# Kernel optimization log

Hardware: AMD Instinct MI355X
Metric: run time of the kernel (lower is better)

The kernel has to match this reference:

```python
import jax, jax.numpy as jnp
import numpy as np

B, N, D, A = 4, 4096, 512, 64

def setup_inputs() -> dict:
    key = jax.random.key(0)
    ks = jax.random.split(key, 7)
    s = 1.0 / np.sqrt(D)
    return {
        "inputs": jax.random.normal(ks[0], (B, N, D), dtype=jnp.float32),
        "Wq": jax.random.normal(ks[1], (D, A), dtype=jnp.float32) * s,
        "bq": jnp.zeros((A,), dtype=jnp.float32),
        "Wk": jax.random.normal(ks[2], (D, A), dtype=jnp.float32) * s,
        "bk": jnp.zeros((A,), dtype=jnp.float32),
        "Wv": jax.random.normal(ks[3], (D, A), dtype=jnp.float32) * s,
        "bv": jnp.zeros((A,), dtype=jnp.float32),
    }

def reference(inputs, Wq, bq, Wk, bk, Wv, bv):
    # Dense projections: [B,N,D] @ [D,A] + [A] -> [B,N,A]
    Q = jnp.einsum('bnd,da->bna', inputs, Wq) + bq
    K = jnp.einsum('bnd,da->bna', inputs, Wk) + bk
    V = jnp.einsum('bnd,da->bna', inputs, Wv) + bv
    scale = 1.0 / jnp.sqrt(jnp.float32(A))
    scores = jnp.einsum('bqa,bka->bqk', Q, K) * scale  # [B,N,N]
    weights = jax.nn.softmax(scores, axis=-1)
    return jnp.einsum('bqk,bka->bqa', weights, V)  # [B,N,A]
```

## Files before the change

kernel.cpp:

```cpp
#include <hip/hip_runtime.h>
#include <hip/hip_bf16.h>

namespace {

constexpr int Bn = 4, Nn = 4096, An = 64;

typedef __attribute__((ext_vector_type(8))) short bf16x8;
typedef __attribute__((ext_vector_type(4))) float f32x4;

constexpr float QSCALE = 0.125f * 1.4426950408889634f;

__device__ __forceinline__ short f2bf(float f) {
    __hip_bfloat16 h = __float2bfloat16(f);
    return *reinterpret_cast<short*>(&h);
}
__device__ __forceinline__ float bf2f(short s) {
    unsigned u = ((unsigned)(unsigned short)s) << 16;
    return *reinterpret_cast<float*>(&u);
}
__device__ __forceinline__ unsigned cvt_pk_bf16(float a, float b) {
    unsigned r;
    asm("v_cvt_pk_bf16_f32 %0, %1, %2" : "=v"(r) : "v"(a), "v"(b));
    return r;
}
__device__ __forceinline__ float hw_exp2(float x) {
    return __builtin_amdgcn_exp2f(x);
}

__global__ __launch_bounds__(256) void wpack(
    const float* __restrict__ Wq, const float* __restrict__ bq,
    const float* __restrict__ Wk, const float* __restrict__ bk,
    const float* __restrict__ Wv, const float* __restrict__ bv,
    short* __restrict__ Wt, float* __restrict__ bc)
{
    const int tid = blockIdx.x * 256 + threadIdx.x;
    const int c = tid >> 6, k0 = (tid & 63) << 3;
    const int m = c >> 6, a = c & 63;
    const float* W = (m == 0) ? Wq : (m == 1) ? Wk : Wv;
    const float s = (m == 0) ? QSCALE : 1.0f;
    bf16x8 o;
    #pragma unroll
    for (int j = 0; j < 8; ++j) o[j] = f2bf(W[(size_t)(k0 + j) * 64 + a] * s);
    *reinterpret_cast<bf16x8*>(Wt + (size_t)c * 512 + k0) = o;
    if (tid < 192) bc[tid] = (m == 0) ? bq[a] * QSCALE : (m == 1) ? bk[a] : bv[a];
}

__global__ __launch_bounds__(512, 4) void qkv_mm(
    const float* __restrict__ x, const short* __restrict__ Wt,
    const float* __restrict__ bc,
    __hip_bfloat16* __restrict__ Qb, __hip_bfloat16* __restrict__ Kb,
    __hip_bfloat16* __restrict__ Vt)
{
    __shared__ __align__(16) short wls[64 * 512];

    const int tid  = threadIdx.x;
    const int w    = tid >> 6, lane = tid & 63;
    const int lo   = lane & 15, g = lane >> 4;
    const int rowgrp = blockIdx.x / 3;
    const int colgrp = blockIdx.x - rowgrp * 3;
    const int r0   = rowgrp * 128;
    const int c0   = colgrp * 64;

    {
        const uint4* wsrc = reinterpret_cast<const uint4*>(Wt + (size_t)c0 * 512);
        uint4* wdst = reinterpret_cast<uint4*>(wls);
        #pragma unroll
        for (int i = 0; i < 8; ++i) {
            int idx = i * 512 + tid;
            int c = idx >> 6, slot = idx & 63;
            wdst[c * 64 + (slot ^ (c & 7))] = wsrc[idx];
        }
    }
    __syncthreads();

    const int myrow = r0 + w * 16 + lo;
    const float* xr = x + (size_t)myrow * 512 + 8 * g;

    f32x4 acc[4];
    #pragma unroll
    for (int i = 0; i < 4; ++i) acc[i] = f32x4{0.f, 0.f, 0.f, 0.f};

    #pragma unroll 4
    for (int kt = 0; kt < 512; kt += 32) {
        float4 a0 = *reinterpret_cast<const float4*>(xr + kt);
        float4 a1 = *reinterpret_cast<const float4*>(xr + kt + 4);
        float xf[8] = {a0.x, a0.y, a0.z, a0.w, a1.x, a1.y, a1.z, a1.w};
        uint4 hv;
        hv.x = cvt_pk_bf16(xf[0], xf[1]); hv.y = cvt_pk_bf16(xf[2], xf[3]);
        hv.z = cvt_pk_bf16(xf[4], xf[5]); hv.w = cvt_pk_bf16(xf[6], xf[7]);
        bf16x8 ah = *reinterpret_cast<bf16x8*>(&hv);
        float rs[8];
        #pragma unroll
        for (int j = 0; j < 8; ++j) rs[j] = xf[j] - bf2f(ah[j]);
        uint4 lv;
        lv.x = cvt_pk_bf16(rs[0], rs[1]); lv.y = cvt_pk_bf16(rs[2], rs[3]);
        lv.z = cvt_pk_bf16(rs[4], rs[5]); lv.w = cvt_pk_bf16(rs[6], rs[7]);
        bf16x8 al = *reinterpret_cast<bf16x8*>(&lv);

        const int slot = (kt >> 3) + g;
        #pragma unroll
        for (int ct = 0; ct < 4; ++ct) {
            int c = ct * 16 + lo;
            const bf16x8 wf = *reinterpret_cast<const bf16x8*>(
                wls + c * 512 + ((slot ^ (c & 7)) << 3));
            acc[ct] = __builtin_amdgcn_mfma_f32_16x16x32_bf16(ah, wf, acc[ct], 0, 0, 0);
            acc[ct] = __builtin_amdgcn_mfma_f32_16x16x32_bf16(al, wf, acc[ct], 0, 0, 0);
        }
    }

    const int bb = r0 >> 12;
    if (colgrp < 2) {
        __hip_bfloat16* dst = (colgrp == 0) ? Qb : Kb;
        #pragma unroll
        for (int ct = 0; ct < 4; ++ct) {
            const float bias = bc[c0 + ct * 16 + lo];
            #pragma unroll
            for (int r = 0; r < 4; ++r) {
                short hv2 = f2bf(acc[ct][r] + bias);
                dst[(size_t)(r0 + w * 16 + 4 * g + r) * 64 + ct * 16 + lo] =
                    *reinterpret_cast<__hip_bfloat16*>(&hv2);
            }
        }
    } else {
        __syncthreads();
        short* vt = wls + w * 1024;
        #pragma unroll
        for (int ct = 0; ct < 4; ++ct) {
            const float bias = bc[128 + ct * 16 + lo];
            #pragma unroll
            for (int r = 0; r < 4; ++r)
                vt[(4 * g + r) * 64 + ct * 16 + lo] = f2bf(acc[ct][r] + bias);
        }
        asm volatile("s_waitcnt lgkmcnt(0)" ::: "memory");
        __builtin_amdgcn_sched_barrier(0);
        unsigned u[8];
        #pragma unroll
        for (int n = 0; n < 8; ++n) {
            unsigned v0 = (unsigned short)vt[(2 * n) * 64 + lane];
            unsigned v1 = (unsigned short)vt[(2 * n + 1) * 64 + lane];
            u[n] = v0 | (v1 << 16);
        }
        const int n0w = (r0 & 4095) + w * 16;
        uint4* dstv = reinterpret_cast<uint4*>(&Vt[((size_t)(bb * 64 + lane)) * 4096 + n0w]);
        dstv[0] = uint4{u[0], u[1], u[2], u[3]};
        dstv[1] = uint4{u[4], u[5], u[6], u[7]};
    }
}

template<int WAVES, int KS, bool DIRECT>
__global__ __launch_bounds__(WAVES * 64, 2) void attn(
    const __hip_bfloat16* __restrict__ Qb,
    const __hip_bfloat16* __restrict__ Kb,
    const __hip_bfloat16* __restrict__ Vt,
    float* __restrict__ Pacc, float* __restrict__ Lbuf, float* __restrict__ outD)
{
    constexpr int T    = WAVES * 64;
    constexpr int QPB  = WAVES * 32;
    constexpr int SBPB = Nn / QPB;
    constexpr int NC   = 512 / T;

    __shared__ __align__(16) short Klds[2][64 * 64];
    __shared__ __align__(16) short Vlds[2][64 * 64];
    __shared__ __align__(16) short Plds[WAVES][2][16 * 64];

    const int tid  = threadIdx.x;
    const int w    = tid >> 6, lane = tid & 63;
    const int lo   = lane & 15, g = lane >> 4;
    const int qsb  = blockIdx.x / KS;
    const int ks   = blockIdx.x % KS;
    const int b    = qsb / SBPB;
    const int nqb  = (qsb % SBPB) * QPB;
    const int k0b  = ks * (Nn / KS);
    const int nsteps = (Nn / KS) / 64;

    bf16x8 qf[2][2];
    #pragma unroll
    for (int qt = 0; qt < 2; ++qt)
        #pragma unroll
        for (int dh = 0; dh < 2; ++dh)
            qf[qt][dh] = *reinterpret_cast<const bf16x8*>(
                &Qb[(size_t)(b * Nn + nqb + w * 32 + qt * 16 + lo) * 64 + dh * 32 + 8 * g]);

    f32x4 acc[2][4];
    #pragma unroll
    for (int q = 0; q < 2; ++q)
        #pragma unroll
        for (int a = 0; a < 4; ++a) acc[q][a] = f32x4{0.f, 0.f, 0.f, 0.f};
    float lsum[2] = {0.f, 0.f};

    uint4 kr[NC], vr[NC];
    auto stg_issue = [&](int s) {
        int k0 = k0b + s * 64;
        #pragma unroll
        for (int i = 0; i < NC; ++i) {
            int c = i * T + tid, key = c >> 3, sl = c & 7;
            kr[i] = *reinterpret_cast<const uint4*>(&Kb[(size_t)(b * Nn + k0 + key) * 64 + sl * 8]);
            vr[i] = *reinterpret_cast<const uint4*>(&Vt[(size_t)(b * 64 + key) * Nn + k0 + sl * 8]);
        }
    };
    auto stg_write = [&](int buf) {
        #pragma unroll
        for (int i = 0; i < NC; ++i) {
            int c = i * T + tid, key = c >> 3, ss = (c & 7) ^ (key & 7);
            *reinterpret_cast<uint4*>(&Klds[buf][key * 64 + ss * 8]) = kr[i];
            *reinterpret_cast<uint4*>(&Vlds[buf][key * 64 + ss * 8]) = vr[i];
        }
    };

    auto step = [&](int buf) {
        bf16x8 ka[4][2], va[4][2];
        #pragma unroll
        for (int t = 0; t < 4; ++t)
            #pragma unroll
            for (int dh = 0; dh < 2; ++dh) {
                int row = lo + 16 * t, ss = (g + 4 * dh) ^ (row & 7);
                ka[t][dh] = *reinterpret_cast<const bf16x8*>(&Klds[buf][row * 64 + ss * 8]);
            }
        #pragma unroll
        for (int at = 0; at < 4; ++at)
            #pragma unroll
            for (int c = 0; c < 2; ++c) {
                int row = at * 16 + lo, ss = (4 * c + g) ^ (row & 7);
                va[at][c] = *reinterpret_cast<const bf16x8*>(&Vlds[buf][row * 64 + ss * 8]);
            }

        f32x4 cc[2][4];
        #pragma unroll
        for (int qt = 0; qt < 2; ++qt)
            #pragma unroll
            for (int t = 0; t < 4; ++t) {
                f32x4 c = f32x4{0.f, 0.f, 0.f, 0.f};
                c = __builtin_amdgcn_mfma_f32_16x16x32_bf16(ka[t][0], qf[qt][0], c, 0, 0, 0);
                c = __builtin_amdgcn_mfma_f32_16x16x32_bf16(ka[t][1], qf[qt][1], c, 0, 0, 0);
                cc[qt][t] = c;
            }

        #pragma unroll
        for (int qt = 0; qt < 2; ++qt) {
            char* pbase = reinterpret_cast<char*>(&Plds[w][qt][0]) + lo * 128;
            #pragma unroll
            for (int t = 0; t < 4; ++t) {
                float p0 = hw_exp2(cc[qt][t][0]), p1 = hw_exp2(cc[qt][t][1]);
                float p2 = hw_exp2(cc[qt][t][2]), p3 = hw_exp2(cc[qt][t][3]);
                lsum[qt] += (p0 + p1) + (p2 + p3);
                uint2 pw = {cvt_pk_bf16(p0, p1), cvt_pk_bf16(p2, p3)};
                int byte = (32 * t + 8 * g) ^ ((lo & 7) << 4);
                *reinterpret_cast<uint2*>(pbase + byte) = pw;
            }
        }
        asm volatile("s_waitcnt lgkmcnt(0)" ::: "memory");

        #pragma unroll
        for (int qt = 0; qt < 2; ++qt) {
            char* pbase = reinterpret_cast<char*>(&Plds[w][qt][0]) + lo * 128;
            bf16x8 pb[2];
            #pragma unroll
            for (int c = 0; c < 2; ++c) {
                int byte = (64 * c + 16 * g) ^ ((lo & 7) << 4);
                pb[c] = *reinterpret_cast<const bf16x8*>(pbase + byte);
            }
            #pragma unroll
            for (int at = 0; at < 4; ++at) {
                acc[qt][at] = __builtin_amdgcn_mfma_f32_16x16x32_bf16(va[at][0], pb[0], acc[qt][at], 0, 0, 0);
                acc[qt][at] = __builtin_amdgcn_mfma_f32_16x16x32_bf16(va[at][1], pb[1], acc[qt][at], 0, 0, 0);
            }
        }
    };

    stg_issue(0);
    stg_write(0);
    __syncthreads();
    for (int s = 0; s < nsteps; ++s) {
        if (s + 1 < nsteps) stg_issue(s + 1);
        step(s & 1);
        if (s + 1 < nsteps) {
            stg_write((s + 1) & 1);
            __syncthreads();
        }
    }

    #pragma unroll
    for (int qt = 0; qt < 2; ++qt) {
        float l = lsum[qt];
        l += __shfl_xor(l, 16);
        l += __shfl_xor(l, 32);
        const int n = nqb + w * 32 + qt * 16 + lo;
        if (!DIRECT) {
            if (g == 0) Lbuf[(size_t)(ks * Bn + b) * Nn + n] = l;
            #pragma unroll
            for (int at = 0; at < 4; ++at)
                #pragma unroll
                for (int r = 0; r < 4; ++r) {
                    int a = at * 16 + 4 * g + r;
                    Pacc[((size_t)(ks * Bn + b) * An + a) * Nn + n] = acc[qt][at][r];
                }
        } else {
            float inv = 1.0f / l;
            #pragma unroll
            for (int at = 0; at < 4; ++at)
                #pragma unroll
                for (int r = 0; r < 4; ++r)
                    outD[((size_t)(b * Nn) + n) * 64 + at * 16 + 4 * g + r] = acc[qt][at][r] * inv;
        }
    }
}

__global__ __launch_bounds__(256) void reduce_out(
    const float* __restrict__ Pacc, const float* __restrict__ Lbuf,
    float* __restrict__ out, int KS)
{
    __shared__ float sa[64][65];
    __shared__ float sl[64];
    const int b = blockIdx.x >> 6, n0 = (blockIdx.x & 63) * 64;
    const int t = threadIdx.x;

    float r[16];
    #pragma unroll
    for (int i = 0; i < 16; ++i) r[i] = 0.f;
    for (int s = 0; s < KS; ++s) {
        const float* P = Pacc + (size_t)(s * Bn + b) * An * Nn;
        #pragma unroll
        for (int i = 0; i < 16; ++i) {
            int idx = i * 256 + t;
            r[i] += P[(size_t)(idx >> 6) * Nn + n0 + (idx & 63)];
        }
    }
    #pragma unroll
    for (int i = 0; i < 16; ++i) { int idx = i * 256 + t; sa[idx >> 6][idx & 63] = r[i]; }
    if (t < 64) {
        float lv = 0.f;
        for (int s = 0; s < KS; ++s) lv += Lbuf[(size_t)(s * Bn + b) * Nn + n0 + t];
        sl[t] = 1.0f / lv;
    }
    __syncthreads();
    #pragma unroll
    for (int i = 0; i < 4; ++i) {
        int chunk = i * 256 + t, row = chunk >> 4, c4 = chunk & 15;
        float inv = sl[row];
        float4 v;
        v.x = sa[c4 * 4 + 0][row] * inv;
        v.y = sa[c4 * 4 + 1][row] * inv;
        v.z = sa[c4 * 4 + 2][row] * inv;
        v.w = sa[c4 * 4 + 3][row] * inv;
        *reinterpret_cast<float4*>(&out[((size_t)b * Nn + n0 + row) * 64 + c4 * 4]) = v;
    }
}

}

extern "C" void kernel_launch(void* const* d_in, const int* in_sizes, int n_in,
                              void* d_out, int out_size, void* d_ws, size_t ws_size,
                              hipStream_t stream) {
    const float* x  = (const float*)d_in[0];
    const float* Wq = (const float*)d_in[1];
    const float* bq = (const float*)d_in[2];
    const float* Wk = (const float*)d_in[3];
    const float* bk = (const float*)d_in[4];
    const float* Wv = (const float*)d_in[5];
    const float* bv = (const float*)d_in[6];
    float* out = (float*)d_out;

    char* ws = (char*)d_ws;
    const size_t mat_bytes = (size_t)Bn * Nn * An * sizeof(__hip_bfloat16);
    __hip_bfloat16* Qb = (__hip_bfloat16*)(ws);
    __hip_bfloat16* Kb = (__hip_bfloat16*)(ws + mat_bytes);
    __hip_bfloat16* Vt = (__hip_bfloat16*)(ws + 2 * mat_bytes);
    float* Pacc = (float*)(ws + 3 * mat_bytes);
    const size_t pacc_bytes = (size_t)Bn * An * Nn * sizeof(float);
    const size_t lbuf_per   = (size_t)Bn * Nn * sizeof(float);

    short* Wt = (short*)d_out;
    float* bc = (float*)((char*)d_out + 192 * 512 * 2);

    wpack<<<dim3(48), dim3(256), 0, stream>>>(Wq, bq, Wk, bk, Wv, bv, Wt, bc);
    qkv_mm<<<dim3(384), dim3(512), 0, stream>>>(x, Wt, bc, Qb, Kb, Vt);

    const size_t base = 3 * mat_bytes;
    if (ws_size >= base + 4 * (pacc_bytes + lbuf_per)) {
        float* Lbuf = (float*)(ws + base + 4 * pacc_bytes);
        attn<8, 4, false><<<dim3((Bn * Nn / 256) * 4), dim3(512), 0, stream>>>(Qb, Kb, Vt, Pacc, Lbuf, out);
        reduce_out<<<dim3(256), dim3(256), 0, stream>>>(Pacc, Lbuf, out, 4);
    } else if (ws_size >= base + 2 * (pacc_bytes + lbuf_per)) {
        float* Lbuf = (float*)(ws + base + 2 * pacc_bytes);
        attn<4, 2, false><<<dim3((Bn * Nn / 128) * 2), dim3(256), 0, stream>>>(Qb, Kb, Vt, Pacc, Lbuf, out);
        reduce_out<<<dim3(256), dim3(256), 0, stream>>>(Pacc, Lbuf, out, 2);
    } else {
        attn<4, 1, true><<<dim3(Bn * Nn / 128), dim3(256), 0, stream>>>(Qb, Kb, Vt, nullptr, nullptr, out);
    }
}
```

Measured before the change: 59.75 us.

## Load K and V fragments directly from global memory, dropping LDS staging

Removes the double-buffered LDS staging of K and V tiles along with the per-step block barriers. Each wave now loads its MFMA operand fragments for K and V straight from global memory (through L1/L2), with the V loads issued after the exp/P writes. This cuts LDS traffic, LDS footprint and __syncthreads overhead. In exchange, every wave in a block re-fetches the same K/V data from cache, and the loads are no longer prefetched a step ahead, so global latency may be exposed.

```diff
diff --git a/kernel.cpp b/kernel.cpp
--- a/kernel.cpp
+++ b/kernel.cpp
@@ -154,13 +154,10 @@
     const __hip_bfloat16* __restrict__ Vt,
     float* __restrict__ Pacc, float* __restrict__ Lbuf, float* __restrict__ outD)
 {
-    constexpr int T    = WAVES * 64;
     constexpr int QPB  = WAVES * 32;
     constexpr int SBPB = Nn / QPB;
-    constexpr int NC   = 512 / T;
-
-    __shared__ __align__(16) short Klds[2][64 * 64];
-    __shared__ __align__(16) short Vlds[2][64 * 64];
+    constexpr int NSTEPS = (Nn / KS) / 64;
+
     __shared__ __align__(16) short Plds[WAVES][2][16 * 64];
 
     const int tid  = threadIdx.x;
@@ -171,7 +168,6 @@
     const int b    = qsb / SBPB;
     const int nqb  = (qsb % SBPB) * QPB;
     const int k0b  = ks * (Nn / KS);
-    const int nsteps = (Nn / KS) / 64;
 
     bf16x8 qf[2][2];
     #pragma unroll
@@ -188,41 +184,19 @@
         for (int a = 0; a < 4; ++a) acc[q][a] = f32x4{0.f, 0.f, 0.f, 0.f};
     float lsum[2] = {0.f, 0.f};
 
-    uint4 kr[NC], vr[NC];
-    auto stg_issue = [&](int s) {
-        int k0 = k0b + s * 64;
-        #pragma unroll
-        for (int i = 0; i < NC; ++i) {
-            int c = i * T + tid, key = c >> 3, sl = c & 7;
-            kr[i] = *reinterpret_cast<const uint4*>(&Kb[(size_t)(b * Nn + k0 + key) * 64 + sl * 8]);
-            vr[i] = *reinterpret_cast<const uint4*>(&Vt[(size_t)(b * 64 + key) * Nn + k0 + sl * 8]);
-        }
-    };
-    auto stg_write = [&](int buf) {
-        #pragma unroll
-        for (int i = 0; i < NC; ++i) {
-            int c = i * T + tid, key = c >> 3, ss = (c & 7) ^ (key & 7);
-            *reinterpret_cast<uint4*>(&Klds[buf][key * 64 + ss * 8]) = kr[i];
-            *reinterpret_cast<uint4*>(&Vlds[buf][key * 64 + ss * 8]) = vr[i];
-        }
-    };
-
-    auto step = [&](int buf) {
-        bf16x8 ka[4][2], va[4][2];
+    const __hip_bfloat16* Kbp = Kb + (size_t)b * Nn * 64;
+    const __hip_bfloat16* Vbp = Vt + (size_t)b * 64 * Nn;
+
+    for (int s = 0; s < NSTEPS; ++s) {
+        const int kt = k0b + s * 64;
+
+        bf16x8 ka[4][2];
         #pragma unroll
         for (int t = 0; t < 4; ++t)
             #pragma unroll
-            for (int dh = 0; dh < 2; ++dh) {
-                int row = lo + 16 * t, ss = (g + 4 * dh) ^ (row & 7);
-                ka[t][dh] = *reinterpret_cast<const bf16x8*>(&Klds[buf][row * 64 + ss * 8]);
-            }
-        #pragma unroll
-        for (int at = 0; at < 4; ++at)
-            #pragma unroll
-            for (int c = 0; c < 2; ++c) {
-                int row = at * 16 + lo, ss = (4 * c + g) ^ (row & 7);
-                va[at][c] = *reinterpret_cast<const bf16x8*>(&Vlds[buf][row * 64 + ss * 8]);
-            }
+            for (int dh = 0; dh < 2; ++dh)
+                ka[t][dh] = *reinterpret_cast<const bf16x8*>(
+                    &Kbp[(size_t)(kt + 16 * t + lo) * 64 + dh * 32 + 8 * g]);
 
         f32x4 cc[2][4];
         #pragma unroll
@@ -248,6 +222,15 @@
                 *reinterpret_cast<uint2*>(pbase + byte) = pw;
             }
         }
+
+        bf16x8 va[4][2];
+        #pragma unroll
+        for (int at = 0; at < 4; ++at)
+            #pragma unroll
+            for (int c = 0; c < 2; ++c)
+                va[at][c] = *reinterpret_cast<const bf16x8*>(
+                    &Vbp[(size_t)(16 * at + lo) * 4096 + kt + 32 * c + 8 * g]);
+
         asm volatile("s_waitcnt lgkmcnt(0)" ::: "memory");
 
         #pragma unroll
@@ -264,18 +247,6 @@
                 acc[qt][at] = __builtin_amdgcn_mfma_f32_16x16x32_bf16(va[at][0], pb[0], acc[qt][at], 0, 0, 0);
                 acc[qt][at] = __builtin_amdgcn_mfma_f32_16x16x32_bf16(va[at][1], pb[1], acc[qt][at], 0, 0, 0);
             }
-        }
-    };
-
-    stg_issue(0);
-    stg_write(0);
-    __syncthreads();
-    for (int s = 0; s < nsteps; ++s) {
-        if (s + 1 < nsteps) stg_issue(s + 1);
-        step(s & 1);
-        if (s + 1 < nsteps) {
-            stg_write((s + 1) & 1);
-            __syncthreads();
         }
     }
 
```

New measurement: 97.13 us. 1.63x slower.
